# Optimization experiments

Measured on AMD Instinct MI355X. Metric: run time of the kernel, lower is better.

## Reference

```python
import jax, jax.numpy as jnp
import numpy as np

B, L, S, H, E, D = 2, 2048, 2048, 16, 64, 64

def setup_inputs() -> dict:
    key = jax.random.key(0)
    kq, kk, kv = jax.random.split(key, 3)
    queries = jax.random.normal(kq, (B, L, H, E), dtype=jnp.float32)
    keys = jax.random.normal(kk, (B, S, H, E), dtype=jnp.float32)
    values = jax.random.normal(kv, (B, S, H, D), dtype=jnp.float32)
    mask = jnp.zeros((1, 1, L, S), dtype=jnp.float32)  # additive mask, broadcast over B,H
    return {"queries": queries, "keys": keys, "values": values, "mask": mask}

def reference(queries, keys, values, mask):
    # scale defaults to 1/sqrt(E)
    scale = 1.0 / jnp.sqrt(jnp.asarray(queries.shape[-1], queries.dtype))
    # scores: [B,H,L,S]
    scores = jnp.einsum('blhe,bshe->bhls', queries, keys)
    scores = scores + mask
    A = jax.nn.softmax(scale * scores, axis=-1)  # dropout rate 0 => identity
    V = jnp.einsum('bhls,bshd->blhd', A, values)
    return V
```

## Files before the change

### kernel.cpp

```cpp
#include <hip/hip_runtime.h>

typedef _Float16 half8 __attribute__((ext_vector_type(8)));
typedef _Float16 half4 __attribute__((ext_vector_type(4)));
typedef float f32x4 __attribute__((ext_vector_type(4)));

constexpr int B = 2, L = 2048, S = 2048, H = 16, E = 64, D = 64;
constexpr int BM = 128;
constexpr int BN = 64;
constexpr int LDT = 72;
constexpr int NTI = S / BN;

__global__ __launch_bounds__(256, 2)
void fa_kernel(const float* __restrict__ Qg, const float* __restrict__ Kg,
               const float* __restrict__ Vg, const float* __restrict__ Mg,
               float* __restrict__ Og)
{
    __shared__ _Float16 sK[BN][LDT];
    __shared__ _Float16 sV[D][LDT];
    __shared__ _Float16 sP[4][32][LDT];

    const int tid  = threadIdx.x;
    const int wave = tid >> 6;
    const int lane = tid & 63;
    const int quad = lane >> 4;
    const int lq   = lane & 15;

    const int i  = blockIdx.x;
    const int bh = (i & 7) * 4 + ((i >> 3) & 3);
    const int qb = i >> 5;
    const int b  = bh >> 4;
    const int h  = bh & 15;
    const int q0 = qb * BM;

    const int rowStride = H * E;
    const size_t qbase = ((size_t)b * L) * rowStride + h * E;
    const size_t kbase = ((size_t)b * S) * rowStride + h * E;

    const float cS = 0.125f * 1.44269504089f;

    half8 qf[2][2];
    #pragma unroll
    for (int g = 0; g < 2; ++g) {
        const float* qp = Qg + qbase + (size_t)(q0 + wave*32 + g*16 + lq) * rowStride + quad*8;
        #pragma unroll
        for (int ks = 0; ks < 2; ++ks)
            #pragma unroll
            for (int j = 0; j < 8; ++j)
                qf[g][ks][j] = (_Float16)(qp[ks*32 + j] * cS);
    }

    const float* mrow0 = Mg + (size_t)(q0 + wave*32 + lq) * S;

    float lsum[2] = {0.f, 0.f};
    f32x4 oacc[2][4];
    #pragma unroll
    for (int g = 0; g < 2; ++g)
        #pragma unroll
        for (int dt = 0; dt < 4; ++dt) oacc[g][dt] = (f32x4){0.f, 0.f, 0.f, 0.f};

    const int db = tid & 15;
    const int sb = tid >> 4;
    const float* vbase = Vg + kbase + (size_t)(sb*4) * rowStride + db*4;
    const float* krow  = Kg + kbase + (size_t)(tid >> 4) * rowStride + (tid & 15)*4;
    const int voff = (((sb >> 1) ^ (db >> 1)) << 3) + ((sb & 1) << 2);

    float4 kreg[4], vreg[4], mreg[2][4];

    #pragma unroll
    for (int ii = 0; ii < 4; ++ii)
        kreg[ii] = *(const float4*)(krow + (size_t)(ii*16) * rowStride);
    #pragma unroll
    for (int j = 0; j < 4; ++j)
        vreg[j] = *(const float4*)(vbase + (size_t)j * rowStride);
    #pragma unroll
    for (int g = 0; g < 2; ++g)
        #pragma unroll
        for (int nt = 0; nt < 4; ++nt)
            mreg[g][nt] = *(const float4*)(mrow0 + (size_t)g*16*S + nt*16 + quad*4);

    #pragma unroll
    for (int ii = 0; ii < 4; ++ii) {
        half4 hk = {(_Float16)kreg[ii].x, (_Float16)kreg[ii].y,
                    (_Float16)kreg[ii].z, (_Float16)kreg[ii].w};
        *(half4*)&sK[(tid >> 4) + ii*16][(tid & 15)*4] = hk;
    }
    #pragma unroll
    for (int j = 0; j < 4; ++j) {
        half4 hv = { (_Float16)((&vreg[0].x)[j]), (_Float16)((&vreg[1].x)[j]),
                     (_Float16)((&vreg[2].x)[j]), (_Float16)((&vreg[3].x)[j]) };
        *(half4*)&sV[db*4 + j][voff] = hv;
    }
    __syncthreads();

    for (int t = 0; t < NTI; ++t) {
        if (t + 1 < NTI) {
            const int s1 = (t + 1) * BN;
            #pragma unroll
            for (int ii = 0; ii < 4; ++ii)
                kreg[ii] = *(const float4*)(krow + (size_t)(s1 + ii*16) * rowStride);
            #pragma unroll
            for (int j = 0; j < 4; ++j)
                vreg[j] = *(const float4*)(vbase + (size_t)(s1 + j) * rowStride);
        }

        f32x4 sf[2][4];
        __builtin_amdgcn_s_setprio(1);
        #pragma unroll
        for (int nt = 0; nt < 4; ++nt) {
            half8 kf0 = *(const half8*)&sK[nt*16 + lq][ 0 + quad*8];
            half8 kf1 = *(const half8*)&sK[nt*16 + lq][32 + quad*8];
            #pragma unroll
            for (int g = 0; g < 2; ++g) {
                f32x4 acc = (f32x4){0.f, 0.f, 0.f, 0.f};
                acc = __builtin_amdgcn_mfma_f32_16x16x32_f16(kf0, qf[g][0], acc, 0, 0, 0);
                acc = __builtin_amdgcn_mfma_f32_16x16x32_f16(kf1, qf[g][1], acc, 0, 0, 0);
                sf[g][nt] = acc;
            }
        }
        __builtin_amdgcn_s_setprio(0);

        #pragma unroll
        for (int g = 0; g < 2; ++g)
            #pragma unroll
            for (int nt = 0; nt < 4; ++nt) {
                half4 hp;
                #pragma unroll
                for (int r = 0; r < 4; ++r) {
                    float lg = fmaf((&mreg[g][nt].x)[r], cS, sf[g][nt][r]);
                    float p  = __builtin_amdgcn_exp2f(lg);
                    lsum[g] += p;
                    hp[r] = (_Float16)p;
                }
                *(half4*)&sP[wave][g*16 + lq][nt*16 + quad*4] = hp;
            }

        if (t + 1 < NTI) {
            const int s1 = (t + 1) * BN;
            #pragma unroll
            for (int g = 0; g < 2; ++g)
                #pragma unroll
                for (int nt = 0; nt < 4; ++nt)
                    mreg[g][nt] = *(const float4*)(mrow0 + (size_t)g*16*S + s1 + nt*16 + quad*4);
        }

        __builtin_amdgcn_s_setprio(1);
        #pragma unroll
        for (int ks = 0; ks < 2; ++ks) {
            half8 pf0 = *(const half8*)&sP[wave][ 0 + lq][ks*32 + quad*8];
            half8 pf1 = *(const half8*)&sP[wave][16 + lq][ks*32 + quad*8];
            #pragma unroll
            for (int dt = 0; dt < 4; ++dt) {
                const int vrow = dt*16 + lq;
                const int phys = (ks*4 + quad) ^ ((vrow >> 3) & 7);
                half8 vf = *(const half8*)&sV[vrow][phys << 3];
                oacc[0][dt] = __builtin_amdgcn_mfma_f32_16x16x32_f16(pf0, vf, oacc[0][dt], 0, 0, 0);
                oacc[1][dt] = __builtin_amdgcn_mfma_f32_16x16x32_f16(pf1, vf, oacc[1][dt], 0, 0, 0);
            }
        }
        __builtin_amdgcn_s_setprio(0);

        if (t + 1 < NTI) {
            __syncthreads();
            #pragma unroll
            for (int ii = 0; ii < 4; ++ii) {
                half4 hk = {(_Float16)kreg[ii].x, (_Float16)kreg[ii].y,
                            (_Float16)kreg[ii].z, (_Float16)kreg[ii].w};
                *(half4*)&sK[(tid >> 4) + ii*16][(tid & 15)*4] = hk;
            }
            #pragma unroll
            for (int j = 0; j < 4; ++j) {
                half4 hv = { (_Float16)((&vreg[0].x)[j]), (_Float16)((&vreg[1].x)[j]),
                             (_Float16)((&vreg[2].x)[j]), (_Float16)((&vreg[3].x)[j]) };
                *(half4*)&sV[db*4 + j][voff] = hv;
            }
            __syncthreads();
        }
    }

    #pragma unroll
    for (int g = 0; g < 2; ++g) {
        float l = lsum[g];
        l += __shfl_xor(l, 16);
        l += __shfl_xor(l, 32);
        #pragma unroll
        for (int r = 0; r < 4; ++r) {
            float l_bc = __shfl(l, quad*4 + r, 16);
            float inv = 1.f / l_bc;
            float* orow = Og + qbase + (size_t)(q0 + wave*32 + g*16 + quad*4 + r) * rowStride;
            #pragma unroll
            for (int dt = 0; dt < 4; ++dt)
                orow[dt*16 + lq] = oacc[g][dt][r] * inv;
        }
    }
}

extern "C" void kernel_launch(void* const* d_in, const int* in_sizes, int n_in,
                              void* d_out, int out_size, void* d_ws, size_t ws_size,
                              hipStream_t stream) {
    const float* Qg = (const float*)d_in[0];
    const float* Kg = (const float*)d_in[1];
    const float* Vg = (const float*)d_in[2];
    const float* Mg = (const float*)d_in[3];
    float* Og = (float*)d_out;
    dim3 grid((L / BM) * B * H);
    fa_kernel<<<grid, 256, 0, stream>>>(Qg, Kg, Vg, Mg, Og);
}
```

Before: 177.0 us.

## Pre-convert K, transposed V and mask to fp16 in workspace, read fragments directly

Adds a prep kernel that writes K as fp16 (per-head contiguous), V transposed to fp16, and the mask pre-scaled to fp16 into the workspace buffer. The main attention kernel then loads MFMA fragments straight from global memory into registers, double-buffered across tiles through a macro, with no LDS staging for K and V and no block-wide barriers. The P scratch buffer in LDS now uses an XOR swizzle instead of padding. This trades an extra launch and a workspace round trip for removing LDS conversion stores and syncs. The old kernel is kept as a fallback when no workspace is available.

```diff
diff --git a/kernel.cpp b/kernel.cpp
--- a/kernel.cpp
+++ b/kernel.cpp
@@ -7,17 +7,157 @@
 constexpr int B = 2, L = 2048, S = 2048, H = 16, E = 64, D = 64;
 constexpr int BM = 128;
 constexpr int BN = 64;
-constexpr int LDT = 72;
 constexpr int NTI = S / BN;
+constexpr float CS = 0.125f * 1.44269504089f;
+
+constexpr size_t KH_HALFS = (size_t)B * H * S * E;
+constexpr size_t VT_HALFS = (size_t)B * H * D * S;
+constexpr size_t MH_HALFS = (size_t)L * S;
+constexpr size_t WS_NEED  = (KH_HALFS + VT_HALFS + MH_HALFS) * 2;
+
+__global__ __launch_bounds__(256, 4)
+void prep_kernel(const float* __restrict__ Kg, const float* __restrict__ Vg,
+                 const float* __restrict__ Mg, _Float16* __restrict__ ws)
+{
+    _Float16* Kh  = ws;
+    _Float16* VTh = ws + KH_HALFS;
+    _Float16* Mh  = ws + KH_HALFS + VT_HALFS;
+    const int tid = threadIdx.x;
+    const int bid = blockIdx.x;
+
+    if (bid < 4096) {
+        const int idx = bid * 256 + tid;
+        const int e   = (idx & 15) * 4;
+        const int s   = (idx >> 4) & 2047;
+        const int hb  = idx >> 15;
+        const int h   = hb & 15, b = hb >> 4;
+        const float4 v = *(const float4*)(Kg + ((size_t)(b * S + s)) * (H * E) + h * E + e);
+        half4 o = {(_Float16)v.x, (_Float16)v.y, (_Float16)v.z, (_Float16)v.w};
+        *(half4*)(Kh + ((size_t)((b * H + h) * S + s)) * E + e) = o;
+    } else if (bid < 8192) {
+        const size_t idx = (size_t)(bid - 4096) * 256 + tid;
+        const float4 v = *(const float4*)(Mg + idx * 4);
+        half4 o = {(_Float16)(v.x * CS), (_Float16)(v.y * CS),
+                   (_Float16)(v.z * CS), (_Float16)(v.w * CS)};
+        *(half4*)(Mh + idx * 4) = o;
+    } else {
+        __shared__ _Float16 tile[64][68];
+        const int bid2 = bid - 8192;
+        const int sblk = bid2 & 31;
+        const int h    = (bid2 >> 5) & 15;
+        const int b    = bid2 >> 9;
+        const int ts = tid >> 4, d4 = (tid & 15) << 2;
+        #pragma unroll
+        for (int ii = 0; ii < 4; ++ii) {
+            const int s = sblk * 64 + ts + ii * 16;
+            const float4 v = *(const float4*)(Vg + ((size_t)(b * S + s)) * (H * D) + h * D + d4);
+            #pragma unroll
+            for (int j = 0; j < 4; ++j)
+                tile[d4 + j][ts + ii * 16] = (_Float16)((&v.x)[j]);
+        }
+        __syncthreads();
+        const int d = tid >> 2, sc = (tid & 3) << 4;
+        #pragma unroll
+        for (int c = 0; c < 4; ++c) {
+            half4 o;
+            #pragma unroll
+            for (int k = 0; k < 4; ++k) o[k] = tile[d][sc + c * 4 + k];
+            *(half4*)(VTh + ((size_t)((b * H + h) * D + d) << 11) + sblk * 64 + sc + c * 4) = o;
+        }
+    }
+}
+
+
+#define TILE_STEP(KC, KN, MC, MN, T)                                                        \
+{                                                                                           \
+    const int s0_ = (T) * BN;                                                               \
+                  \
+    _Pragma("unroll")                                                                       \
+    for (int ks = 0; ks < 2; ++ks)                                                          \
+        _Pragma("unroll")                                                                   \
+        for (int dt = 0; dt < 4; ++dt)                                                      \
+            vfr[ks*4+dt] = *(const half8*)(vt_bh + ((size_t)(dt*16 + lq) << 11)             \
+                                           + s0_ + ks*32 + quad*8);                         \
+                                                        \
+    f32x4 sf[2][4];                                                                         \
+    __builtin_amdgcn_s_setprio(1);                                                          \
+    _Pragma("unroll")                                                                       \
+    for (int nt = 0; nt < 4; ++nt) {                                                        \
+        _Pragma("unroll")                                                                   \
+        for (int g = 0; g < 2; ++g) {                                                       \
+            f32x4 acc = (f32x4){0.f, 0.f, 0.f, 0.f};                                        \
+            acc = __builtin_amdgcn_mfma_f32_16x16x32_f16(KC[nt*2+0], qf[g][0], acc, 0,0,0); \
+            acc = __builtin_amdgcn_mfma_f32_16x16x32_f16(KC[nt*2+1], qf[g][1], acc, 0,0,0); \
+            sf[g][nt] = acc;                                                                \
+        }                                                                                   \
+    }                                                                                       \
+    __builtin_amdgcn_s_setprio(0);                                                          \
+                               \
+    if ((T) + 1 < NTI) {                                                                    \
+        const int s1_ = s0_ + BN;                                                           \
+        _Pragma("unroll")                                                                   \
+        for (int nt = 0; nt < 4; ++nt)                                                      \
+            _Pragma("unroll")                                                               \
+            for (int eh = 0; eh < 2; ++eh)                                                  \
+                KN[nt*2+eh] = *(const half8*)(kh_bh + ((size_t)(s1_ + nt*16 + lq) << 6)     \
+                                              + eh*32 + quad*8);                            \
+    }                                                                                       \
+                     \
+    _Pragma("unroll")                                                                       \
+    for (int g = 0; g < 2; ++g) {                                                           \
+        const int row = g*16 + lq;                                                          \
+        char* prow = (char*)&sP[wave][row][0];                                              \
+        _Pragma("unroll")                                                                   \
+        for (int nt = 0; nt < 4; ++nt) {                                                    \
+            half4 hp;                                                                       \
+            _Pragma("unroll")                                                               \
+            for (int r = 0; r < 4; ++r) {                                                   \
+                float lg = sf[g][nt][r] + (float)MC[g*4+nt][r];                             \
+                float p  = __builtin_amdgcn_exp2f(lg);                                      \
+                lsum[g] += p;                                                               \
+                hp[r] = (_Float16)p;                                                        \
+            }                                                                               \
+            *(half4*)(prow + ((((2*nt + (quad>>1)) ^ (lq&7)) << 4) + ((quad&1) << 3))) = hp;\
+        }                                                                                   \
+    }                                                                                       \
+                         \
+    if ((T) + 1 < NTI) {                                                                    \
+        const int s1_ = s0_ + BN;                                                           \
+        _Pragma("unroll")                                                                   \
+        for (int g = 0; g < 2; ++g)                                                         \
+            _Pragma("unroll")                                                               \
+            for (int nt = 0; nt < 4; ++nt)                                                  \
+                MN[g*4+nt] = *(const half4*)(mrow0 + ((size_t)g << 15)                      \
+                                             + s1_ + nt*16 + quad*4);                       \
+    }                                                                                       \
+                                   \
+    __builtin_amdgcn_s_setprio(1);                                                          \
+    _Pragma("unroll")                                                                       \
+    for (int ks = 0; ks < 2; ++ks) {                                                        \
+        half8 pf0 = *(const half8*)((char*)&sP[wave][     lq][0]                            \
+                                    + (((4*ks + quad) ^ (lq&7)) << 4));                     \
+        half8 pf1 = *(const half8*)((char*)&sP[wave][16 + lq][0]                            \
+                                    + (((4*ks + quad) ^ (lq&7)) << 4));                     \
+        _Pragma("unroll")                                                                   \
+        for (int dt = 0; dt < 4; ++dt) {                                                    \
+            oacc[0][dt] = __builtin_amdgcn_mfma_f32_16x16x32_f16(pf0, vfr[ks*4+dt],         \
+                                                                 oacc[0][dt], 0,0,0);       \
+            oacc[1][dt] = __builtin_amdgcn_mfma_f32_16x16x32_f16(pf1, vfr[ks*4+dt],         \
+                                                                 oacc[1][dt], 0,0,0);       \
+        }                                                                                   \
+    }                                                                                       \
+    __builtin_amdgcn_s_setprio(0);                                                          \
+}
 
 __global__ __launch_bounds__(256, 2)
-void fa_kernel(const float* __restrict__ Qg, const float* __restrict__ Kg,
-               const float* __restrict__ Vg, const float* __restrict__ Mg,
-               float* __restrict__ Og)
+void fa2_kernel(const float* __restrict__ Qg, const _Float16* __restrict__ ws,
+                float* __restrict__ Og)
 {
-    __shared__ _Float16 sK[BN][LDT];
-    __shared__ _Float16 sV[D][LDT];
-    __shared__ _Float16 sP[4][32][LDT];
+    __shared__ _Float16 sP[4][32][64];
+
+    const _Float16* Kh  = ws;
+    const _Float16* VTh = ws + KH_HALFS;
+    const _Float16* Mh  = ws + KH_HALFS + VT_HALFS;
 
     const int tid  = threadIdx.x;
     const int wave = tid >> 6;
@@ -34,9 +174,10 @@
 
     const int rowStride = H * E;
     const size_t qbase = ((size_t)b * L) * rowStride + h * E;
-    const size_t kbase = ((size_t)b * S) * rowStride + h * E;
-
-    const float cS = 0.125f * 1.44269504089f;
+
+    const _Float16* kh_bh = Kh  + ((size_t)(b * H + h) << 17);
+    const _Float16* vt_bh = VTh + ((size_t)(b * H + h) << 17);
+    const _Float16* mrow0 = Mh  + ((size_t)(q0 + wave * 32 + lq) << 11);
 
     half8 qf[2][2];
     #pragma unroll
@@ -46,7 +187,89 @@
         for (int ks = 0; ks < 2; ++ks)
             #pragma unroll
             for (int j = 0; j < 8; ++j)
-                qf[g][ks][j] = (_Float16)(qp[ks*32 + j] * cS);
+                qf[g][ks][j] = (_Float16)(qp[ks*32 + j] * CS);
+    }
+
+    float lsum[2] = {0.f, 0.f};
+    f32x4 oacc[2][4];
+    #pragma unroll
+    for (int g = 0; g < 2; ++g)
+        #pragma unroll
+        for (int dt = 0; dt < 4; ++dt) oacc[g][dt] = (f32x4){0.f, 0.f, 0.f, 0.f};
+
+    half8 kfA[8], kfB[8], vfr[8];
+    half4 mA[8], mB[8];
+
+    #pragma unroll
+    for (int nt = 0; nt < 4; ++nt)
+        #pragma unroll
+        for (int eh = 0; eh < 2; ++eh)
+            kfA[nt*2+eh] = *(const half8*)(kh_bh + ((size_t)(nt*16 + lq) << 6) + eh*32 + quad*8);
+    #pragma unroll
+    for (int g = 0; g < 2; ++g)
+        #pragma unroll
+        for (int nt = 0; nt < 4; ++nt)
+            mA[g*4+nt] = *(const half4*)(mrow0 + ((size_t)g << 15) + nt*16 + quad*4);
+
+    for (int tt = 0; tt < NTI; tt += 2) {
+        TILE_STEP(kfA, kfB, mA, mB, tt);
+        TILE_STEP(kfB, kfA, mB, mA, tt + 1);
+    }
+
+    #pragma unroll
+    for (int g = 0; g < 2; ++g) {
+        float l = lsum[g];
+        l += __shfl_xor(l, 16);
+        l += __shfl_xor(l, 32);
+        #pragma unroll
+        for (int r = 0; r < 4; ++r) {
+            float l_bc = __shfl(l, quad*4 + r, 16);
+            float inv = 1.f / l_bc;
+            float* orow = Og + qbase + (size_t)(q0 + wave*32 + g*16 + quad*4 + r) * rowStride;
+            #pragma unroll
+            for (int dt = 0; dt < 4; ++dt)
+                orow[dt*16 + lq] = oacc[g][dt][r] * inv;
+        }
+    }
+}
+
+constexpr int LDT = 72;
+
+__global__ __launch_bounds__(256, 2)
+void fa_fb_kernel(const float* __restrict__ Qg, const float* __restrict__ Kg,
+                  const float* __restrict__ Vg, const float* __restrict__ Mg,
+                  float* __restrict__ Og)
+{
+    __shared__ _Float16 sK[BN][LDT];
+    __shared__ _Float16 sV[D][LDT];
+    __shared__ _Float16 sP[4][32][LDT];
+
+    const int tid  = threadIdx.x;
+    const int wave = tid >> 6;
+    const int lane = tid & 63;
+    const int quad = lane >> 4;
+    const int lq   = lane & 15;
+
+    const int i  = blockIdx.x;
+    const int bh = (i & 7) * 4 + ((i >> 3) & 3);
+    const int qb = i >> 5;
+    const int b  = bh >> 4;
+    const int h  = bh & 15;
+    const int q0 = qb * BM;
+
+    const int rowStride = H * E;
+    const size_t qbase = ((size_t)b * L) * rowStride + h * E;
+    const size_t kbase = ((size_t)b * S) * rowStride + h * E;
+
+    half8 qf[2][2];
+    #pragma unroll
+    for (int g = 0; g < 2; ++g) {
+        const float* qp = Qg + qbase + (size_t)(q0 + wave*32 + g*16 + lq) * rowStride + quad*8;
+        #pragma unroll
+        for (int ks = 0; ks < 2; ++ks)
+            #pragma unroll
+            for (int j = 0; j < 8; ++j)
+                qf[g][ks][j] = (_Float16)(qp[ks*32 + j] * CS);
     }
 
     const float* mrow0 = Mg + (size_t)(q0 + wave*32 + lq) * S;
@@ -126,7 +349,7 @@
                 half4 hp;
                 #pragma unroll
                 for (int r = 0; r < 4; ++r) {
-                    float lg = fmaf((&mreg[g][nt].x)[r], cS, sf[g][nt][r]);
+                    float lg = fmaf((&mreg[g][nt].x)[r], CS, sf[g][nt][r]);
                     float p  = __builtin_amdgcn_exp2f(lg);
                     lsum[g] += p;
                     hp[r] = (_Float16)p;
@@ -202,6 +425,12 @@
     const float* Vg = (const float*)d_in[2];
     const float* Mg = (const float*)d_in[3];
     float* Og = (float*)d_out;
-    dim3 grid((L / BM) * B * H);
-    fa_kernel<<<grid, 256, 0, stream>>>(Qg, Kg, Vg, Mg, Og);
+
+    if (ws_size >= WS_NEED && d_ws != nullptr) {
+        _Float16* ws = (_Float16*)d_ws;
+        prep_kernel<<<dim3(4096 + 4096 + 1024), 256, 0, stream>>>(Kg, Vg, Mg, ws);
+        fa2_kernel<<<dim3((L / BM) * B * H), 256, 0, stream>>>(Qg, ws, Og);
+    } else {
+        fa_fb_kernel<<<dim3((L / BM) * B * H), 256, 0, stream>>>(Qg, Kg, Vg, Mg, Og);
+    }
 }
```

After: 274.4 us. 55.0% more time.

## Double-buffer K/V shared tiles to drop one barrier per iteration

Applied to the files above, without the earlier changes.

Shared K and V tiles become two buffers. Each step computes from one buffer while writing the next tile into the other, so each tile step needs only one __syncthreads instead of two. The loop is unrolled by two through a macro that alternates the buffers and ping-pongs the mask registers. This raises LDS use per block, which could affect occupancy at two blocks per CU, and adds register pressure from the second mask array.

```diff
diff --git a/kernel.cpp b/kernel.cpp
--- a/kernel.cpp
+++ b/kernel.cpp
@@ -10,13 +10,101 @@
 constexpr int LDT = 72;
 constexpr int NTI = S / BN;
 
+#define TILE_STEP(BUF, MC, MN, T)                                                           \
+{                                                                                           \
+                         \
+    if ((T) + 1 < NTI) {                                                                    \
+        const int s1 = ((T) + 1) * BN;                                                      \
+        _Pragma("unroll")                                                                   \
+        for (int ii = 0; ii < 4; ++ii)                                                      \
+            kreg[ii] = *(const float4*)(krow + (size_t)(s1 + ii*16) * rowStride);           \
+        _Pragma("unroll")                                                                   \
+        for (int j = 0; j < 4; ++j)                                                         \
+            vreg[j] = *(const float4*)(vbase + (size_t)(s1 + j) * rowStride);               \
+    }                                                                                       \
+                     \
+    f32x4 sf[2][4];                                                                         \
+    __builtin_amdgcn_s_setprio(1);                                                          \
+    _Pragma("unroll")                                                                       \
+    for (int nt = 0; nt < 4; ++nt) {                                                        \
+        half8 kf0 = *(const half8*)&sK[BUF][nt*16 + lq][ 0 + quad*8];                       \
+        half8 kf1 = *(const half8*)&sK[BUF][nt*16 + lq][32 + quad*8];                       \
+        _Pragma("unroll")                                                                   \
+        for (int g = 0; g < 2; ++g) {                                                       \
+            f32x4 acc = (f32x4){0.f, 0.f, 0.f, 0.f};                                        \
+            acc = __builtin_amdgcn_mfma_f32_16x16x32_f16(kf0, qf[g][0], acc, 0, 0, 0);      \
+            acc = __builtin_amdgcn_mfma_f32_16x16x32_f16(kf1, qf[g][1], acc, 0, 0, 0);      \
+            sf[g][nt] = acc;                                                                \
+        }                                                                                   \
+    }                                                                                       \
+    __builtin_amdgcn_s_setprio(0);                                                          \
+                      \
+    _Pragma("unroll")                                                                       \
+    for (int g = 0; g < 2; ++g)                                                             \
+        _Pragma("unroll")                                                                   \
+        for (int nt = 0; nt < 4; ++nt) {                                                    \
+            half4 hp;                                                                       \
+            _Pragma("unroll")                                                               \
+            for (int r = 0; r < 4; ++r) {                                                   \
+                float lg = fmaf((&MC[g][nt].x)[r], cS, sf[g][nt][r]);                       \
+                float p  = __builtin_amdgcn_exp2f(lg);                                      \
+                lsum[g] += p;                                                               \
+                hp[r] = (_Float16)p;                                                        \
+            }                                                                               \
+            *(half4*)&sP[wave][g*16 + lq][nt*16 + quad*4] = hp;                             \
+        }                                                                                   \
+                                                  \
+    if ((T) + 1 < NTI) {                                                                    \
+        const int s1 = ((T) + 1) * BN;                                                      \
+        _Pragma("unroll")                                                                   \
+        for (int g = 0; g < 2; ++g)                                                         \
+            _Pragma("unroll")                                                               \
+            for (int nt = 0; nt < 4; ++nt)                                                  \
+                MN[g][nt] = *(const float4*)(mrow0 + (size_t)g*16*S + s1 + nt*16 + quad*4); \
+    }                                                                                       \
+                                            \
+    __builtin_amdgcn_s_setprio(1);                                                          \
+    _Pragma("unroll")                                                                       \
+    for (int ks = 0; ks < 2; ++ks) {                                                        \
+        half8 pf0 = *(const half8*)&sP[wave][ 0 + lq][ks*32 + quad*8];                      \
+        half8 pf1 = *(const half8*)&sP[wave][16 + lq][ks*32 + quad*8];                      \
+        _Pragma("unroll")                                                                   \
+        for (int dt = 0; dt < 4; ++dt) {                                                    \
+            const int vrow = dt*16 + lq;                                                    \
+            const int phys = (ks*4 + quad) ^ ((vrow >> 3) & 7);                             \
+            half8 vf = *(const half8*)&sV[BUF][vrow][phys << 3];                            \
+            oacc[0][dt] = __builtin_amdgcn_mfma_f32_16x16x32_f16(pf0, vf, oacc[0][dt],0,0,0);\
+            oacc[1][dt] = __builtin_amdgcn_mfma_f32_16x16x32_f16(pf1, vf, oacc[1][dt],0,0,0);\
+        }                                                                                   \
+    }                                                                                       \
+    __builtin_amdgcn_s_setprio(0);                                                          \
+                    \
+    if ((T) + 1 < NTI) {                                                                    \
+        _Pragma("unroll")                                                                   \
+        for (int ii = 0; ii < 4; ++ii) {                                                    \
+            half4 hk = {(_Float16)kreg[ii].x, (_Float16)kreg[ii].y,                         \
+                        (_Float16)kreg[ii].z, (_Float16)kreg[ii].w};                        \
+            *(half4*)&sK[(BUF) ^ 1][(tid >> 4) + ii*16][(tid & 15)*4] = hk;                 \
+        }                                                                                   \
+        _Pragma("unroll")                                                                   \
+        for (int j = 0; j < 4; ++j) {                                                       \
+            half4 hv = { (_Float16)((&kvx(0))[j]), (_Float16)((&kvx(1))[j]),                \
+                         (_Float16)((&kvx(2))[j]), (_Float16)((&kvx(3))[j]) };              \
+            *(half4*)&sV[(BUF) ^ 1][db*4 + j][voff] = hv;                                   \
+        }                                                                                   \
+        __syncthreads();  \
+    }                                                                                       \
+}
+
+#define kvx(n) vreg[n].x
+
 __global__ __launch_bounds__(256, 2)
 void fa_kernel(const float* __restrict__ Qg, const float* __restrict__ Kg,
                const float* __restrict__ Vg, const float* __restrict__ Mg,
                float* __restrict__ Og)
 {
-    __shared__ _Float16 sK[BN][LDT];
-    __shared__ _Float16 sV[D][LDT];
+    __shared__ _Float16 sK[2][BN][LDT];
+    __shared__ _Float16 sV[2][D][LDT];
     __shared__ _Float16 sP[4][32][LDT];
 
     const int tid  = threadIdx.x;
@@ -64,7 +152,7 @@
     const float* krow  = Kg + kbase + (size_t)(tid >> 4) * rowStride + (tid & 15)*4;
     const int voff = (((sb >> 1) ^ (db >> 1)) << 3) + ((sb & 1) << 2);
 
-    float4 kreg[4], vreg[4], mreg[2][4];
+    float4 kreg[4], vreg[4], mA[2][4], mB[2][4];
 
     #pragma unroll
     for (int ii = 0; ii < 4; ++ii)
@@ -76,105 +164,25 @@
     for (int g = 0; g < 2; ++g)
         #pragma unroll
         for (int nt = 0; nt < 4; ++nt)
-            mreg[g][nt] = *(const float4*)(mrow0 + (size_t)g*16*S + nt*16 + quad*4);
+            mA[g][nt] = *(const float4*)(mrow0 + (size_t)g*16*S + nt*16 + quad*4);
 
     #pragma unroll
     for (int ii = 0; ii < 4; ++ii) {
         half4 hk = {(_Float16)kreg[ii].x, (_Float16)kreg[ii].y,
                     (_Float16)kreg[ii].z, (_Float16)kreg[ii].w};
-        *(half4*)&sK[(tid >> 4) + ii*16][(tid & 15)*4] = hk;
+        *(half4*)&sK[0][(tid >> 4) + ii*16][(tid & 15)*4] = hk;
     }
     #pragma unroll
     for (int j = 0; j < 4; ++j) {
         half4 hv = { (_Float16)((&vreg[0].x)[j]), (_Float16)((&vreg[1].x)[j]),
                      (_Float16)((&vreg[2].x)[j]), (_Float16)((&vreg[3].x)[j]) };
-        *(half4*)&sV[db*4 + j][voff] = hv;
+        *(half4*)&sV[0][db*4 + j][voff] = hv;
     }
     __syncthreads();
 
-    for (int t = 0; t < NTI; ++t) {
-        if (t + 1 < NTI) {
-            const int s1 = (t + 1) * BN;
-            #pragma unroll
-            for (int ii = 0; ii < 4; ++ii)
-                kreg[ii] = *(const float4*)(krow + (size_t)(s1 + ii*16) * rowStride);
-            #pragma unroll
-            for (int j = 0; j < 4; ++j)
-                vreg[j] = *(const float4*)(vbase + (size_t)(s1 + j) * rowStride);
-        }
-
-        f32x4 sf[2][4];
-        __builtin_amdgcn_s_setprio(1);
-        #pragma unroll
-        for (int nt = 0; nt < 4; ++nt) {
-            half8 kf0 = *(const half8*)&sK[nt*16 + lq][ 0 + quad*8];
-            half8 kf1 = *(const half8*)&sK[nt*16 + lq][32 + quad*8];
-            #pragma unroll
-            for (int g = 0; g < 2; ++g) {
-                f32x4 acc = (f32x4){0.f, 0.f, 0.f, 0.f};
-                acc = __builtin_amdgcn_mfma_f32_16x16x32_f16(kf0, qf[g][0], acc, 0, 0, 0);
-                acc = __builtin_amdgcn_mfma_f32_16x16x32_f16(kf1, qf[g][1], acc, 0, 0, 0);
-                sf[g][nt] = acc;
-            }
-        }
-        __builtin_amdgcn_s_setprio(0);
-
-        #pragma unroll
-        for (int g = 0; g < 2; ++g)
-            #pragma unroll
-            for (int nt = 0; nt < 4; ++nt) {
-                half4 hp;
-                #pragma unroll
-                for (int r = 0; r < 4; ++r) {
-                    float lg = fmaf((&mreg[g][nt].x)[r], cS, sf[g][nt][r]);
-                    float p  = __builtin_amdgcn_exp2f(lg);
-                    lsum[g] += p;
-                    hp[r] = (_Float16)p;
-                }
-                *(half4*)&sP[wave][g*16 + lq][nt*16 + quad*4] = hp;
-            }
-
-        if (t + 1 < NTI) {
-            const int s1 = (t + 1) * BN;
-            #pragma unroll
-            for (int g = 0; g < 2; ++g)
-                #pragma unroll
-                for (int nt = 0; nt < 4; ++nt)
-                    mreg[g][nt] = *(const float4*)(mrow0 + (size_t)g*16*S + s1 + nt*16 + quad*4);
-        }
-
-        __builtin_amdgcn_s_setprio(1);
-        #pragma unroll
-        for (int ks = 0; ks < 2; ++ks) {
-            half8 pf0 = *(const half8*)&sP[wave][ 0 + lq][ks*32 + quad*8];
-            half8 pf1 = *(const half8*)&sP[wave][16 + lq][ks*32 + quad*8];
-            #pragma unroll
-            for (int dt = 0; dt < 4; ++dt) {
-                const int vrow = dt*16 + lq;
-                const int phys = (ks*4 + quad) ^ ((vrow >> 3) & 7);
-                half8 vf = *(const half8*)&sV[vrow][phys << 3];
-                oacc[0][dt] = __builtin_amdgcn_mfma_f32_16x16x32_f16(pf0, vf, oacc[0][dt], 0, 0, 0);
-                oacc[1][dt] = __builtin_amdgcn_mfma_f32_16x16x32_f16(pf1, vf, oacc[1][dt], 0, 0, 0);
-            }
-        }
-        __builtin_amdgcn_s_setprio(0);
-
-        if (t + 1 < NTI) {
-            __syncthreads();
-            #pragma unroll
-            for (int ii = 0; ii < 4; ++ii) {
-                half4 hk = {(_Float16)kreg[ii].x, (_Float16)kreg[ii].y,
-                            (_Float16)kreg[ii].z, (_Float16)kreg[ii].w};
-                *(half4*)&sK[(tid >> 4) + ii*16][(tid & 15)*4] = hk;
-            }
-            #pragma unroll
-            for (int j = 0; j < 4; ++j) {
-                half4 hv = { (_Float16)((&vreg[0].x)[j]), (_Float16)((&vreg[1].x)[j]),
-                             (_Float16)((&vreg[2].x)[j]), (_Float16)((&vreg[3].x)[j]) };
-                *(half4*)&sV[db*4 + j][voff] = hv;
-            }
-            __syncthreads();
-        }
+    for (int tt = 0; tt < NTI; tt += 2) {
+        TILE_STEP(0, mA, mB, tt)
+        TILE_STEP(1, mB, mA, tt + 1)
     }
 
     #pragma unroll
```

Measured after the change: 176.0 us. About the same (-0.6%).
